# Kernel tuning notes

Measured on AMD Instinct MI355X. Metric: run time of the kernel, lower is better.

Reference implementation:

```python
import jax, jax.numpy as jnp
import numpy as np
from jax import lax

SPHERE_RADIUS = 0.05
CHUNK = 2048  # pcd tile size for online-min (avoids materializing full MxN)


def setup_inputs() -> dict:
    key = jax.random.key(0)
    k1, k2 = jax.random.split(key)
    M, N = 65536, 32768
    x = jax.random.normal(k1, (M, 3), dtype=jnp.float32)
    pcd = jax.random.normal(k2, (N, 3), dtype=jnp.float32)
    signs = jnp.ones((M, 1), dtype=jnp.float32)
    return {"x": x, "pcd": pcd, "signs": signs}


def reference(x, pcd, signs):
    # 1-NN squared distance from each query in x (M,3) to the point cloud pcd (N,3),
    # computed as a streaming min over pcd chunks (never materialize MxN).
    M = x.shape[0]
    n_chunks = pcd.shape[0] // CHUNK
    pcd_chunks = pcd.reshape(n_chunks, CHUNK, 3)
    x_sq = jnp.sum(x * x, axis=1)  # (M,)

    def step(best, p):
        p_sq = jnp.sum(p * p, axis=1)                    # (CHUNK,)
        d = x_sq[:, None] + p_sq[None, :] - 2.0 * (x @ p.T)  # (M, CHUNK)
        return jnp.minimum(best, jnp.min(d, axis=1)), None

    init = jnp.full((M,), jnp.inf, dtype=x.dtype)
    best, _ = lax.scan(step, init, pcd_chunks)
    # chamfer returns squared distances; module takes sqrt, subtracts radius, applies signs
    dist = jnp.sqrt(jnp.maximum(best, 0.0))[:, None] - SPHERE_RADIUS  # (M, 1)
    return dist * signs
```

## Files before the change

### kernel.cpp

```cpp
#include <hip/hip_runtime.h>
#include <math.h>

#define RADIUS 0.05f

#define G 64
#define NC (G * G * G)
#define BOXLO -5.5f
#define BOXHI 5.5f
#define CELLH (11.0f / G)
#define INVH (G / 11.0f)
#define R_CAP 2

__device__ __forceinline__ int cell_coord(float v) {
    int c = (int)floorf((v - BOXLO) * INVH);
    return min(G - 1, max(0, c));
}

__global__ void hist_kernel(const float* __restrict__ pcd, unsigned int* __restrict__ cnt, int N) {
    int j = blockIdx.x * 256 + threadIdx.x;
    if (j >= N) return;
    int cx = cell_coord(pcd[3 * j + 0]);
    int cy = cell_coord(pcd[3 * j + 1]);
    int cz = cell_coord(pcd[3 * j + 2]);
    atomicAdd(&cnt[(cx * G + cy) * G + cz], 1u);
}

__global__ void scan1(const unsigned int* __restrict__ cnt, uint2* __restrict__ meta,
                      unsigned int* __restrict__ partials) {
    __shared__ unsigned int s[256];
    int i = blockIdx.x * 256 + threadIdx.x;
    unsigned int v = cnt[i];
    s[threadIdx.x] = v;
    __syncthreads();
    for (int st = 1; st < 256; st <<= 1) {
        unsigned int a = (threadIdx.x >= (unsigned)st) ? s[threadIdx.x - st] : 0u;
        __syncthreads();
        s[threadIdx.x] += a;
        __syncthreads();
    }
    meta[i] = make_uint2(s[threadIdx.x] - v, v);
    if (threadIdx.x == 255) partials[blockIdx.x] = s[255];
}

__global__ void scan2(unsigned int* __restrict__ partials) {
    __shared__ unsigned int s[1024];
    int t = threadIdx.x;
    unsigned int v = partials[t];
    s[t] = v;
    __syncthreads();
    for (int st = 1; st < 1024; st <<= 1) {
        unsigned int a = (t >= st) ? s[t - st] : 0u;
        __syncthreads();
        s[t] += a;
        __syncthreads();
    }
    partials[t] = s[t] - v;
}

__global__ void scan3(uint2* __restrict__ meta, unsigned int* __restrict__ cursor,
                      const unsigned int* __restrict__ partials) {
    int i = blockIdx.x * 256 + threadIdx.x;
    unsigned int off = meta[i].x + partials[blockIdx.x];
    meta[i].x = off;
    cursor[i] = off;
}

__global__ void scatter_kernel(const float* __restrict__ pcd, unsigned int* __restrict__ cursor,
                               float4* __restrict__ pps, int N) {
    int j = blockIdx.x * 256 + threadIdx.x;
    if (j >= N) return;
    float p0 = pcd[3 * j + 0];
    float p1 = pcd[3 * j + 1];
    float p2 = pcd[3 * j + 2];
    int c = (cell_coord(p0) * G + cell_coord(p1)) * G + cell_coord(p2);
    unsigned int idx = atomicAdd(&cursor[c], 1u);
    pps[idx] = make_float4(-2.0f * p0, -2.0f * p1, -2.0f * p2,
                           p0 * p0 + p1 * p1 + p2 * p2);
}

__global__ __launch_bounds__(256) void grid_query_a(const float* __restrict__ x,
                                                    const float* __restrict__ signs,
                                                    const uint2* __restrict__ meta,
                                                    const float4* __restrict__ pps,
                                                    float* __restrict__ out,
                                                    unsigned int* __restrict__ qcount,
                                                    unsigned int* __restrict__ queue, int M) {
    int q = blockIdx.x * 256 + threadIdx.x;
    if (q >= M) return;

    float qx = x[3 * q + 0], qy = x[3 * q + 1], qz = x[3 * q + 2];
    int cx = cell_coord(qx), cy = cell_coord(qy), cz = cell_coord(qz);
    float ov = fmaxf(fmaxf(fmaxf(BOXLO - qx, qx - BOXHI), fmaxf(BOXLO - qy, qy - BOXHI)),
                     fmaxf(fmaxf(BOXLO - qz, qz - BOXHI), 0.0f));
    float xs = fmaf(qx, qx, fmaf(qy, qy, qz * qz));

    float best = INFINITY;
    bool resolved = false;
    for (int r = 0; r <= R_CAP; ++r) {
        for (int dz = -r; dz <= r; ++dz) {
            int z = cz + dz;
            if ((unsigned)z >= (unsigned)G) continue;
            bool face_z = (dz == -r || dz == r);
            for (int dy = -r; dy <= r; ++dy) {
                int y = cy + dy;
                if ((unsigned)y >= (unsigned)G) continue;
                bool face = face_z || (dy == -r || dy == r);
                int step = face ? 1 : 2 * r;
                if (step <= 0) step = 1;
                for (int dx = -r; dx <= r; dx += step) {
                    int xx = cx + dx;
                    if ((unsigned)xx >= (unsigned)G) continue;
                    uint2 mc = meta[(xx * G + y) * G + z];
                    const float4* p = pps + mc.x;
                    unsigned k = 0;
                    for (; k + 2 <= mc.y; k += 2) {
                        float4 a = p[k], b = p[k + 1];
                        float ea = fmaf(a.x, qx, fmaf(a.y, qy, fmaf(a.z, qz, a.w)));
                        float eb = fmaf(b.x, qx, fmaf(b.y, qy, fmaf(b.z, qz, b.w)));
                        best = fminf(best, fminf(ea, eb));
                    }
                    if (k < mc.y) {
                        float4 a = p[k];
                        best = fminf(best, fmaf(a.x, qx, fmaf(a.y, qy, fmaf(a.z, qz, a.w))));
                    }
                }
            }
        }
        float thr = r * CELLH - ov;
        if (thr > 0.0f && best + xs <= thr * thr) { resolved = true; break; }
    }

    if (resolved) {
        float d = fmaxf(xs + best, 0.0f);
        out[q] = (sqrtf(d) - RADIUS) * signs[q];
    } else {
        unsigned int idx = atomicAdd(qcount, 1u);
        queue[idx] = (unsigned int)q;
    }
}

__global__ __launch_bounds__(256) void brute_queue(const float* __restrict__ x,
                                                   const float* __restrict__ signs,
                                                   const float4* __restrict__ pps,
                                                   const unsigned int* __restrict__ qcount,
                                                   const unsigned int* __restrict__ queue,
                                                   float* __restrict__ out, int N) {
    int lane = threadIdx.x & 63;
    int gwave = blockIdx.x * 4 + (threadIdx.x >> 6);
    int nwaves = gridDim.x * 4;
    unsigned int count = *qcount;

    for (unsigned int w = gwave; w < count; w += nwaves) {
        int q = (int)queue[w];
        float qx = x[3 * q + 0], qy = x[3 * q + 1], qz = x[3 * q + 2];
        float e0 = INFINITY, e1 = INFINITY, e2 = INFINITY, e3 = INFINITY;
        int j = lane;
        for (; j + 192 < N; j += 256) {
            float4 a = pps[j], b = pps[j + 64], c = pps[j + 128], d4 = pps[j + 192];
            e0 = fminf(e0, fmaf(a.x, qx, fmaf(a.y, qy, fmaf(a.z, qz, a.w))));
            e1 = fminf(e1, fmaf(b.x, qx, fmaf(b.y, qy, fmaf(b.z, qz, b.w))));
            e2 = fminf(e2, fmaf(c.x, qx, fmaf(c.y, qy, fmaf(c.z, qz, c.w))));
            e3 = fminf(e3, fmaf(d4.x, qx, fmaf(d4.y, qy, fmaf(d4.z, qz, d4.w))));
        }
        for (; j < N; j += 64) {
            float4 a = pps[j];
            e0 = fminf(e0, fmaf(a.x, qx, fmaf(a.y, qy, fmaf(a.z, qz, a.w))));
        }
        float e = fminf(fminf(e0, e1), fminf(e2, e3));
        e = fminf(e, __shfl_xor(e, 1));
        e = fminf(e, __shfl_xor(e, 2));
        e = fminf(e, __shfl_xor(e, 4));
        e = fminf(e, __shfl_xor(e, 8));
        e = fminf(e, __shfl_xor(e, 16));
        e = fminf(e, __shfl_xor(e, 32));
        if (lane == 0) {
            float xsq = fmaf(qx, qx, fmaf(qy, qy, qz * qz));
            float d = fmaxf(xsq + e, 0.0f);
            out[q] = (sqrtf(d) - RADIUS) * signs[q];
        }
    }
}

#define QPT 8
#define NSEG 64
typedef float f32x2 __attribute__((ext_vector_type(2)));

__global__ void init_best(unsigned int* __restrict__ best, int M) {
    int i = blockIdx.x * blockDim.x + threadIdx.x;
    if (i < M) best[i] = 0x7F800000u;
}

__global__ void pack_pcd(const float* __restrict__ pcd, float4* __restrict__ pp, int N) {
    int j = blockIdx.x * blockDim.x + threadIdx.x;
    if (j < N) {
        float p0 = pcd[3 * j], p1 = pcd[3 * j + 1], p2 = pcd[3 * j + 2];
        pp[j] = make_float4(-2.0f * p0, -2.0f * p1, -2.0f * p2,
                            p0 * p0 + p1 * p1 + p2 * p2);
    }
}

__global__ __launch_bounds__(256) void nn_min8(const float* __restrict__ x,
                                               const float4* __restrict__ pp,
                                               unsigned int* __restrict__ best,
                                               int M, int N, int seg_len, int qstride) {
    int t = blockIdx.x * 256 + threadIdx.x;
    int j0 = blockIdx.y * seg_len;
    int j1 = j0 + seg_len;
    if (j1 > N) j1 = N;

    int qid[QPT];
    f32x2 X0[4], X1[4], X2[4], E[4];
#pragma unroll
    for (int r = 0; r < 4; ++r) {
        int q0 = t + (2 * r) * qstride;
        int q1 = t + (2 * r + 1) * qstride;
        qid[2 * r] = q0;
        qid[2 * r + 1] = q1;
        bool ok0 = q0 < M, ok1 = q1 < M;
        int b0 = ok0 ? 3 * q0 : 0;
        int b1 = ok1 ? 3 * q1 : 0;
        X0[r] = (f32x2){ok0 ? x[b0 + 0] : 0.f, ok1 ? x[b1 + 0] : 0.f};
        X1[r] = (f32x2){ok0 ? x[b0 + 1] : 0.f, ok1 ? x[b1 + 1] : 0.f};
        X2[r] = (f32x2){ok0 ? x[b0 + 2] : 0.f, ok1 ? x[b1 + 2] : 0.f};
        E[r] = (f32x2){INFINITY, INFINITY};
    }

#pragma unroll 2
    for (int j = j0; j < j1; ++j) {
        float4 p = pp[j];
        f32x2 px2 = {p.x, p.x};
        f32x2 py2 = {p.y, p.y};
        f32x2 pz2 = {p.z, p.z};
        f32x2 w2 = {p.w, p.w};
#pragma unroll
        for (int r = 0; r < 4; ++r) {
            f32x2 d0 = __builtin_elementwise_fma(pz2, X2[r], w2);
            f32x2 d1 = __builtin_elementwise_fma(py2, X1[r], d0);
            f32x2 d2 = __builtin_elementwise_fma(px2, X0[r], d1);
            E[r].x = fminf(E[r].x, d2.x);
            E[r].y = fminf(E[r].y, d2.y);
        }
    }

#pragma unroll
    for (int r = 0; r < 4; ++r) {
        float xs0 = fmaf(X0[r].x, X0[r].x, fmaf(X1[r].x, X1[r].x, X2[r].x * X2[r].x));
        float xs1 = fmaf(X0[r].y, X0[r].y, fmaf(X1[r].y, X1[r].y, X2[r].y * X2[r].y));
        if (qid[2 * r] < M) {
            float d = fmaxf(xs0 + E[r].x, 0.0f);
            atomicMin(best + qid[2 * r], __float_as_uint(d));
        }
        if (qid[2 * r + 1] < M) {
            float d = fmaxf(xs1 + E[r].y, 0.0f);
            atomicMin(best + qid[2 * r + 1], __float_as_uint(d));
        }
    }
}

__global__ void finalize(unsigned int* __restrict__ bits, const float* __restrict__ signs,
                         float* __restrict__ out, int M) {
    int i = blockIdx.x * blockDim.x + threadIdx.x;
    if (i < M) {
        float d = __uint_as_float(bits[i]);
        out[i] = (sqrtf(d) - RADIUS) * signs[i];
    }
}

extern "C" void kernel_launch(void* const* d_in, const int* in_sizes, int n_in,
                              void* d_out, int out_size, void* d_ws, size_t ws_size,
                              hipStream_t stream) {
    const float* x = (const float*)d_in[0];
    const float* pcd = (const float*)d_in[1];
    const float* signs = (const float*)d_in[2];
    float* out = (float*)d_out;

    int M = in_sizes[0] / 3;
    int N = in_sizes[1] / 3;

    size_t need = (size_t)N * 16 + (size_t)NC * 8 + (size_t)NC * 4 + 4096 + 64 + (size_t)M * 4;

    if (ws_size >= need) {
        char* w = (char*)d_ws;
        float4* pps = (float4*)w;                 w += (size_t)N * 16;
        uint2* meta = (uint2*)w;                  w += (size_t)NC * 8;
        unsigned int* cnt = (unsigned int*)w;     w += (size_t)NC * 4;
        unsigned int* partials = (unsigned int*)w; w += 4096;
        unsigned int* qcount = (unsigned int*)w;  w += 64;
        unsigned int* queue = (unsigned int*)w;
        unsigned int* cursor = cnt;

        hipMemsetAsync(cnt, 0, (size_t)NC * 4, stream);
        hipMemsetAsync(qcount, 0, 4, stream);
        hist_kernel<<<(N + 255) / 256, 256, 0, stream>>>(pcd, cnt, N);
        scan1<<<NC / 256, 256, 0, stream>>>(cnt, meta, partials);
        scan2<<<1, 1024, 0, stream>>>(partials);
        scan3<<<NC / 256, 256, 0, stream>>>(meta, cursor, partials);
        scatter_kernel<<<(N + 255) / 256, 256, 0, stream>>>(pcd, cursor, pps, N);
        grid_query_a<<<(M + 255) / 256, 256, 0, stream>>>(x, signs, meta, pps, out,
                                                          qcount, queue, M);
        brute_queue<<<256, 256, 0, stream>>>(x, signs, pps, qcount, queue, out, N);
    } else {
        float4* pp = (float4*)d_ws;
        init_best<<<(M + 255) / 256, 256, 0, stream>>>((unsigned int*)d_out, M);
        pack_pcd<<<(N + 255) / 256, 256, 0, stream>>>(pcd, pp, N);
        int qstride = (M + QPT - 1) / QPT;
        int seg_len = (N + NSEG - 1) / NSEG;
        dim3 grid((qstride + 255) / 256, NSEG);
        nn_min8<<<grid, 256, 0, stream>>>(x, pp, (unsigned int*)d_out, M, N, seg_len, qstride);
        finalize<<<(M + 255) / 256, 256, 0, stream>>>((unsigned int*)d_out, signs, out, M);
    }
}
```

Measured before the change: 175.8 us.

## Use fixed 27-cell neighborhood with prefetched meta, shuffle scans, larger brute grid

```diff
diff --git a/kernel.cpp b/kernel.cpp
--- a/kernel.cpp
+++ b/kernel.cpp
@@ -9,7 +9,6 @@
 #define BOXHI 5.5f
 #define CELLH (11.0f / G)
 #define INVH (G / 11.0f)
-#define R_CAP 2
 
 __device__ __forceinline__ int cell_coord(float v) {
     int c = (int)floorf((v - BOXLO) * INVH);
@@ -27,34 +26,44 @@
 
 __global__ void scan1(const unsigned int* __restrict__ cnt, uint2* __restrict__ meta,
                       unsigned int* __restrict__ partials) {
-    __shared__ unsigned int s[256];
     int i = blockIdx.x * 256 + threadIdx.x;
     unsigned int v = cnt[i];
-    s[threadIdx.x] = v;
+    unsigned int s = v;
+#pragma unroll
+    for (int off = 1; off < 64; off <<= 1) {
+        unsigned int t = __shfl_up(s, off);
+        if ((threadIdx.x & 63) >= off) s += t;
+    }
+    __shared__ unsigned int wsum[4];
+    int wid = threadIdx.x >> 6;
+    if ((threadIdx.x & 63) == 63) wsum[wid] = s;
     __syncthreads();
-    for (int st = 1; st < 256; st <<= 1) {
-        unsigned int a = (threadIdx.x >= (unsigned)st) ? s[threadIdx.x - st] : 0u;
-        __syncthreads();
-        s[threadIdx.x] += a;
-        __syncthreads();
-    }
-    meta[i] = make_uint2(s[threadIdx.x] - v, v);
-    if (threadIdx.x == 255) partials[blockIdx.x] = s[255];
+    unsigned int base = 0;
+#pragma unroll
+    for (int w = 0; w < 4; ++w)
+        if (w < wid) base += wsum[w];
+    meta[i] = make_uint2(base + s - v, v);
+    if (threadIdx.x == 255) partials[blockIdx.x] = base + s;
 }
 
 __global__ void scan2(unsigned int* __restrict__ partials) {
-    __shared__ unsigned int s[1024];
     int t = threadIdx.x;
     unsigned int v = partials[t];
-    s[t] = v;
+    unsigned int s = v;
+#pragma unroll
+    for (int off = 1; off < 64; off <<= 1) {
+        unsigned int u = __shfl_up(s, off);
+        if ((t & 63) >= off) s += u;
+    }
+    __shared__ unsigned int wsum[16];
+    int wid = t >> 6;
+    if ((t & 63) == 63) wsum[wid] = s;
     __syncthreads();
-    for (int st = 1; st < 1024; st <<= 1) {
-        unsigned int a = (t >= st) ? s[t - st] : 0u;
-        __syncthreads();
-        s[t] += a;
-        __syncthreads();
-    }
-    partials[t] = s[t] - v;
+    unsigned int base = 0;
+#pragma unroll
+    for (int w = 0; w < 16; ++w)
+        if (w < wid) base += wsum[w];
+    partials[t] = base + s - v;
 }
 
 __global__ void scan3(uint2* __restrict__ meta, unsigned int* __restrict__ cursor,
@@ -94,43 +103,39 @@
                      fmaxf(fmaxf(BOXLO - qz, qz - BOXHI), 0.0f));
     float xs = fmaf(qx, qx, fmaf(qy, qy, qz * qz));
 
+    uint2 mc[27];
+#pragma unroll
+    for (int c = 0; c < 27; ++c) {
+        int dxx = c / 9 - 1, dy = (c / 3) % 3 - 1, dz = c % 3 - 1;
+        int X = cx + dxx, Y = cy + dy, Z = cz + dz;
+        bool ok = ((unsigned)X < (unsigned)G) && ((unsigned)Y < (unsigned)G) &&
+                  ((unsigned)Z < (unsigned)G);
+        int idx = ok ? (X * G + Y) * G + Z : 0;
+        uint2 m = meta[idx];
+        mc[c].x = m.x;
+        mc[c].y = ok ? m.y : 0u;
+    }
+
     float best = INFINITY;
-    bool resolved = false;
-    for (int r = 0; r <= R_CAP; ++r) {
-        for (int dz = -r; dz <= r; ++dz) {
-            int z = cz + dz;
-            if ((unsigned)z >= (unsigned)G) continue;
-            bool face_z = (dz == -r || dz == r);
-            for (int dy = -r; dy <= r; ++dy) {
-                int y = cy + dy;
-                if ((unsigned)y >= (unsigned)G) continue;
-                bool face = face_z || (dy == -r || dy == r);
-                int step = face ? 1 : 2 * r;
-                if (step <= 0) step = 1;
-                for (int dx = -r; dx <= r; dx += step) {
-                    int xx = cx + dx;
-                    if ((unsigned)xx >= (unsigned)G) continue;
-                    uint2 mc = meta[(xx * G + y) * G + z];
-                    const float4* p = pps + mc.x;
-                    unsigned k = 0;
-                    for (; k + 2 <= mc.y; k += 2) {
-                        float4 a = p[k], b = p[k + 1];
-                        float ea = fmaf(a.x, qx, fmaf(a.y, qy, fmaf(a.z, qz, a.w)));
-                        float eb = fmaf(b.x, qx, fmaf(b.y, qy, fmaf(b.z, qz, b.w)));
-                        best = fminf(best, fminf(ea, eb));
-                    }
-                    if (k < mc.y) {
-                        float4 a = p[k];
-                        best = fminf(best, fmaf(a.x, qx, fmaf(a.y, qy, fmaf(a.z, qz, a.w))));
-                    }
-                }
-            }
-        }
-        float thr = r * CELLH - ov;
-        if (thr > 0.0f && best + xs <= thr * thr) { resolved = true; break; }
-    }
-
-    if (resolved) {
+#pragma unroll
+    for (int c = 0; c < 27; ++c) {
+        const float4* p = pps + mc[c].x;
+        unsigned n = mc[c].y;
+        unsigned k = 0;
+        for (; k + 2 <= n; k += 2) {
+            float4 a = p[k], b = p[k + 1];
+            float ea = fmaf(a.x, qx, fmaf(a.y, qy, fmaf(a.z, qz, a.w)));
+            float eb = fmaf(b.x, qx, fmaf(b.y, qy, fmaf(b.z, qz, b.w)));
+            best = fminf(best, fminf(ea, eb));
+        }
+        if (k < n) {
+            float4 a = p[k];
+            best = fminf(best, fmaf(a.x, qx, fmaf(a.y, qy, fmaf(a.z, qz, a.w))));
+        }
+    }
+
+    float thr = CELLH - ov;
+    if (thr > 0.0f && best + xs <= thr * thr) {
         float d = fmaxf(xs + best, 0.0f);
         out[q] = (sqrtf(d) - RADIUS) * signs[q];
     } else {
@@ -298,7 +303,7 @@
         scatter_kernel<<<(N + 255) / 256, 256, 0, stream>>>(pcd, cursor, pps, N);
         grid_query_a<<<(M + 255) / 256, 256, 0, stream>>>(x, signs, meta, pps, out,
                                                           qcount, queue, M);
-        brute_queue<<<256, 256, 0, stream>>>(x, signs, pps, qcount, queue, out, N);
+        brute_queue<<<512, 256, 0, stream>>>(x, signs, pps, qcount, queue, out, N);
     } else {
         float4* pp = (float4*)d_ws;
         init_best<<<(M + 255) / 256, 256, 0, stream>>>((unsigned int*)d_out, M);
```

Measured after the change: 181.7 us. 1.03x slower.
